# Performance work log

Measured on AMD Instinct MI355X. Metric: run time of the kernel, lower is better.

## Reference

```python
import jax, jax.numpy as jnp
import numpy as np

D_MODEL = 1024
NUM_HEADS = 16
D_K = D_MODEL // NUM_HEADS


def setup_inputs() -> dict:
    key = jax.random.key(0)
    ks = jax.random.split(key, 9)
    B, S = 4, 2048
    s = 1.0 / np.sqrt(D_MODEL)
    inp = {
        "x": jax.random.normal(ks[0], (B, S, D_MODEL), dtype=jnp.float32),
        "wq": jax.random.uniform(ks[1], (D_MODEL, D_MODEL), jnp.float32, -s, s),
        "bq": jax.random.uniform(ks[2], (D_MODEL,), jnp.float32, -s, s),
        "wk": jax.random.uniform(ks[3], (D_MODEL, D_MODEL), jnp.float32, -s, s),
        "bk": jax.random.uniform(ks[4], (D_MODEL,), jnp.float32, -s, s),
        "wv": jax.random.uniform(ks[5], (D_MODEL, D_MODEL), jnp.float32, -s, s),
        "bv": jax.random.uniform(ks[6], (D_MODEL,), jnp.float32, -s, s),
        "wo": jax.random.uniform(ks[7], (D_MODEL, D_MODEL), jnp.float32, -s, s),
        "bo": jax.random.uniform(ks[8], (D_MODEL,), jnp.float32, -s, s),
    }
    return inp


def reference(x, wq, bq, wk, bk, wv, bv, wo, bo):
    B, S, _ = x.shape
    H, Dk = NUM_HEADS, D_K
    # QKV projections; weights stored as (in, out) so y = x @ w + b
    q = (x @ wq + bq).reshape(B, S, H, Dk).transpose(0, 2, 1, 3)  # (B,H,S,Dk)
    k = (x @ wk + bk).reshape(B, S, H, Dk).transpose(0, 2, 1, 3)
    v = (x @ wv + bv).reshape(B, S, H, Dk).transpose(0, 2, 1, 3)
    scores = jnp.einsum("bhqd,bhkd->bhqk", q, k) / jnp.sqrt(jnp.float32(Dk))
    causal = jnp.tril(jnp.ones((S, S), dtype=bool))  # True = keep
    scores = jnp.where(causal, scores, jnp.float32(-jnp.inf))
    attn = jax.nn.softmax(scores, axis=-1)  # dropout=0 (eval)
    out = jnp.einsum("bhqk,bhkd->bhqd", attn, v)
    out = out.transpose(0, 2, 1, 3).reshape(B, S, H * Dk)
    return out @ wo + bo
```

## Files before the change

kernel.cpp:

```cpp
#include <hip/hip_runtime.h>
#include <hip/hip_bf16.h>


#define D_MODEL 1024
#define NHEADS  16
#define DK      64
#define BATCH   4
#define SEQ     2048
#define MROWS   (BATCH*SEQ)

typedef short bvec8 __attribute__((ext_vector_type(8)));
typedef float fvec4 __attribute__((ext_vector_type(4)));

__device__ __forceinline__ unsigned short f2bf(float f) {
    unsigned int x = __float_as_uint(f);
    x += 0x7fffu + ((x >> 16) & 1u);
    return (unsigned short)(x >> 16);
}

__device__ __forceinline__ unsigned pack_bf16x2(float a, float b) {
#if __has_builtin(__builtin_amdgcn_cvt_pk_bf16_f32)
    typedef __bf16 bf16x2_t __attribute__((ext_vector_type(2)));
    union { bf16x2_t v; unsigned u; } cv;
    cv.v = __builtin_amdgcn_cvt_pk_bf16_f32(a, b);
    return cv.u;
#else
    return (unsigned)f2bf(a) | ((unsigned)f2bf(b) << 16);
#endif
}

__device__ __forceinline__ float fast_exp2(float x) {
#if __has_builtin(__builtin_amdgcn_exp2f)
    return __builtin_amdgcn_exp2f(x);
#else
    return exp2f(x);
#endif
}


__global__ void f32_to_bf16_k(const float* __restrict__ in,
                              unsigned short* __restrict__ out, int n4) {
    int i = blockIdx.x * 256 + threadIdx.x;
    if (i < n4) {
        float4 v = ((const float4*)in)[i];
        ushort4 o;
        o.x = f2bf(v.x); o.y = f2bf(v.y); o.z = f2bf(v.z); o.w = f2bf(v.w);
        ((ushort4*)out)[i] = o;
    }
}

__global__ void transpose_all_k(const float* __restrict__ wq, const float* __restrict__ wk,
                                const float* __restrict__ wv, const float* __restrict__ wo,
                                unsigned short* __restrict__ wqkvt,
                                unsigned short* __restrict__ wot) {
    __shared__ float tile[32][33];
    const int z = blockIdx.z;
    const float* W = (z == 0) ? wq : (z == 1) ? wk : (z == 2) ? wv : wo;
    unsigned short* Wt = (z == 3) ? wot : wqkvt + (size_t)z * D_MODEL * D_MODEL;
    int n0 = blockIdx.x * 32, k0 = blockIdx.y * 32;
    int tx = threadIdx.x & 31;
    int ty = (threadIdx.x >> 5) * 4;
#pragma unroll
    for (int i = 0; i < 4; ++i)
        tile[ty + i][tx] = W[(k0 + ty + i) * D_MODEL + n0 + tx];
    __syncthreads();
#pragma unroll
    for (int i = 0; i < 4; ++i)
        Wt[(n0 + ty + i) * D_MODEL + k0 + tx] = f2bf(tile[tx][ty + i]);
}

__global__ void build_cbias_k(const float* __restrict__ bq, const float* __restrict__ bk,
                              const float* __restrict__ bv, float* __restrict__ cb) {
    int i = blockIdx.x * 256 + threadIdx.x;
    float v = (i < 1024) ? bq[i] : (i < 2048) ? bk[i - 1024] : bv[i - 2048];
    cb[i] = v;
}

__global__ __launch_bounds__(256, 4)
void gemm_glds(const unsigned short* __restrict__ A,
               const unsigned short* __restrict__ Bt,
               const float* __restrict__ bias,
               unsigned short* __restrict__ oq,
               unsigned short* __restrict__ ok,
               unsigned short* __restrict__ ov,
               float* __restrict__ of,
               float qscale, int mode) {
    __shared__ __align__(16) unsigned short As[128 * 64];
    __shared__ __align__(16) unsigned short Bs[128 * 64];

    const int tid  = threadIdx.x;
    const int lane = tid & 63;
    const int w    = tid >> 6;
    const int wr   = w >> 1, wc = w & 1;
    const int quad = lane >> 4, l16 = lane & 15;
    const int rowBlock = blockIdx.y * 128;
    const int colBlock = blockIdx.x * 128;

    const int lrow   = lane >> 3;
    const int gchunk = (lane & 7) ^ lrow;

    fvec4 acc[4][4] = {};

    for (int k0 = 0; k0 < D_MODEL; k0 += 64) {
        __syncthreads();
#pragma unroll
        for (int n = 0; n < 4; ++n) {
            const int g = w * 4 + n;
            const int ra = rowBlock + g * 8 + lrow;
            const int ca = colBlock + g * 8 + lrow;
            __builtin_amdgcn_global_load_lds(
                (const __attribute__((address_space(1))) void*)
                    &A[(size_t)ra * D_MODEL + k0 + gchunk * 8],
                (__attribute__((address_space(3))) void*)&As[g * 512], 16, 0, 0);
            __builtin_amdgcn_global_load_lds(
                (const __attribute__((address_space(1))) void*)
                    &Bt[(size_t)ca * D_MODEL + k0 + gchunk * 8],
                (__attribute__((address_space(3))) void*)&Bs[g * 512], 16, 0, 0);
        }
        __syncthreads();
#pragma unroll
        for (int kc = 0; kc < 2; ++kc) {
            bvec8 af[4], bfr[4];
#pragma unroll
            for (int i = 0; i < 4; ++i) {
                int r = wr * 64 + i * 16 + l16;
                af[i] = *(const bvec8*)&As[r * 64 + (((kc * 4 + quad) ^ (l16 & 7)) * 8)];
            }
#pragma unroll
            for (int j = 0; j < 4; ++j) {
                int r = wc * 64 + j * 16 + l16;
                bfr[j] = *(const bvec8*)&Bs[r * 64 + (((kc * 4 + quad) ^ (l16 & 7)) * 8)];
            }
#pragma unroll
            for (int i = 0; i < 4; ++i)
#pragma unroll
                for (int j = 0; j < 4; ++j)
                    acc[i][j] = __builtin_amdgcn_mfma_f32_16x16x32_bf16(
                        af[i], bfr[j], acc[i][j], 0, 0, 0);
        }
    }

    if (mode == 0) {
#pragma unroll
        for (int i = 0; i < 4; ++i) {
#pragma unroll
            for (int j = 0; j < 4; ++j) {
                int ncol = colBlock + wc * 64 + j * 16 + l16;
                int which = ncol >> 10;
                int nn = ncol & 1023;
                int h = nn >> 6, d = nn & 63;
                float bv = bias[ncol];
#pragma unroll
                for (int r = 0; r < 4; ++r) {
                    int mrow = rowBlock + wr * 64 + i * 16 + quad * 4 + r;
                    int b = mrow >> 11, s = mrow & (SEQ - 1);
                    float v = acc[i][j][r] + bv;
                    if (which == 0)
                        oq[(((b * NHEADS + h) * SEQ + s) * DK) + d] = f2bf(v * qscale);
                    else if (which == 1)
                        ok[(((b * NHEADS + h) * SEQ + s) * DK) + d] = f2bf(v);
                    else
                        ov[(((b * NHEADS + h) * DK + d) * SEQ) + s] = f2bf(v);
                }
            }
        }
    } else {
#pragma unroll
        for (int i = 0; i < 4; ++i) {
#pragma unroll
            for (int j = 0; j < 4; ++j) {
                int ncol = colBlock + wc * 64 + j * 16 + l16;
                float bv = bias[ncol];
#pragma unroll
                for (int r = 0; r < 4; ++r) {
                    int mrow = rowBlock + wr * 64 + i * 16 + quad * 4 + r;
                    of[(size_t)mrow * D_MODEL + ncol] = acc[i][j][r] + bv;
                }
            }
        }
    }
}

__global__ __launch_bounds__(256, 4)
void attn_mfma7(const unsigned short* __restrict__ Q,
                const unsigned short* __restrict__ K,
                const unsigned short* __restrict__ Vt,
                unsigned short* __restrict__ O) {
    __shared__ __align__(16) unsigned short Ksm[2][64 * 64];
    __shared__ __align__(16) unsigned short Vsm[2][64 * 64];
    __shared__ __align__(16) unsigned short Pl[4][32 * 32];

    const int tid  = threadIdx.x;
    const int lane = tid & 63;
    const int wq   = tid >> 6;
    const int quad = lane >> 4, l16 = lane & 15;
    const int bx = blockIdx.x;
    const int qt = (bx & 1) ? ((bx - 1) >> 1) : (15 - (bx >> 1));
    const int h = blockIdx.y, b = blockIdx.z;

    const size_t bhq = ((size_t)b * NHEADS + h) * SEQ * DK;
    const unsigned short* Qb = Q + bhq;
    const unsigned short* Kb = K + bhq;
    const unsigned short* Vb = Vt + bhq;

    const int q0 = qt * 128 + wq * 32;

    bvec8 qf[2][2];
#pragma unroll
    for (int qg = 0; qg < 2; ++qg)
#pragma unroll
        for (int kc = 0; kc < 2; ++kc)
            qf[qg][kc] = *(const bvec8*)&Qb[(q0 + qg * 16 + l16) * DK + kc * 32 + quad * 8];

    const int sr = tid >> 2;
    const int sc = tid & 3;
    const int sp0 = ((sc) ^ (sr & 7)) * 8;
    const int sp1 = ((sc + 4) ^ (sr & 7)) * 8;
    unsigned short* Pw = &Pl[wq][0];

    const int ktmax = 2 * qt + 1;
    const int ktact = 2 * qt + (wq >> 1);
    const int mofs  = (wq & 1) << 5;

    bvec8 kr0, kr1, vr0, vr1;
    {
        const unsigned short* kg = Kb + sr * DK;
        kr0 = *(const bvec8*)(kg + sc * 8);
        kr1 = *(const bvec8*)(kg + (sc + 4) * 8);
        const unsigned short* vg = Vb + sr * SEQ;
        vr0 = *(const bvec8*)(vg + sc * 8);
        vr1 = *(const bvec8*)(vg + (sc + 4) * 8);
        *(bvec8*)&Ksm[0][sr * 64 + sp0] = kr0;
        *(bvec8*)&Ksm[0][sr * 64 + sp1] = kr1;
        *(bvec8*)&Vsm[0][sr * 64 + sp0] = vr0;
        *(bvec8*)&Vsm[0][sr * 64 + sp1] = vr1;
    }

    fvec4 acc[2][4] = {};
    float lp[2] = {0.f, 0.f};

    for (int kt = 0; kt <= ktmax; ++kt) {
        __syncthreads();
        const int buf = kt & 1;
        if (kt < ktmax) {
            const unsigned short* kg = Kb + ((kt + 1) * 64 + sr) * DK;
            kr0 = *(const bvec8*)(kg + sc * 8);
            kr1 = *(const bvec8*)(kg + (sc + 4) * 8);
            const unsigned short* vg = Vb + sr * SEQ + (kt + 1) * 64;
            vr0 = *(const bvec8*)(vg + sc * 8);
            vr1 = *(const bvec8*)(vg + (sc + 4) * 8);
        }
        if (kt <= ktact) {
            const unsigned short* Kbuf = &Ksm[buf][0];
            const unsigned short* Vbuf = &Vsm[buf][0];
#pragma unroll
            for (int half = 0; half < 2; ++half) {
#pragma unroll
                for (int tl = 0; tl < 2; ++tl) {
                    const int t4 = half * 2 + tl;
                    fvec4 s[2] = {};
#pragma unroll
                    for (int kc = 0; kc < 2; ++kc) {
                        bvec8 af = *(const bvec8*)
                            &Kbuf[(t4 * 16 + l16) * 64 + (((kc * 4 + quad) ^ (l16 & 7)) * 8)];
#pragma unroll
                        for (int qg = 0; qg < 2; ++qg)
                            s[qg] = __builtin_amdgcn_mfma_f32_16x16x32_bf16(
                                af, qf[qg][kc], s[qg], 0, 0, 0);
                    }
                    if (kt == ktact) {
#pragma unroll
                        for (int qg = 0; qg < 2; ++qg)
#pragma unroll
                            for (int r = 0; r < 4; ++r) {
                                int key = t4 * 16 + quad * 4 + r - mofs;
                                int qq  = qg * 16 + l16;
                                if (key > qq) s[qg][r] = -__builtin_inff();
                            }
                    }
#pragma unroll
                    for (int qg = 0; qg < 2; ++qg) {
                        float p0 = fast_exp2(s[qg][0]);
                        float p1 = fast_exp2(s[qg][1]);
                        float p2 = fast_exp2(s[qg][2]);
                        float p3 = fast_exp2(s[qg][3]);
                        lp[qg] += (p0 + p1) + (p2 + p3);
                        uint2 pk;
                        pk.x = pack_bf16x2(p0, p1);
                        pk.y = pack_bf16x2(p2, p3);
                        *(uint2*)&Pw[(qg * 16 + l16) * 32 +
                                     (((tl * 2 + (quad >> 1)) ^ (l16 & 3)) * 8) +
                                     (quad & 1) * 4] = pk;
                    }
                }
                bvec8 ap[2];
#pragma unroll
                for (int qg = 0; qg < 2; ++qg)
                    ap[qg] = *(const bvec8*)
                        &Pw[(qg * 16 + l16) * 32 + ((quad ^ (l16 & 3)) * 8)];
#pragma unroll
                for (int dt = 0; dt < 4; ++dt) {
                    bvec8 bv = *(const bvec8*)
                        &Vbuf[(dt * 16 + l16) * 64 + (((half * 4 + quad) ^ (l16 & 7)) * 8)];
#pragma unroll
                    for (int qg = 0; qg < 2; ++qg)
                        acc[qg][dt] = __builtin_amdgcn_mfma_f32_16x16x32_bf16(
                            ap[qg], bv, acc[qg][dt], 0, 0, 0);
                }
            }
        }
        if (kt < ktmax) {
            const int nb = buf ^ 1;
            *(bvec8*)&Ksm[nb][sr * 64 + sp0] = kr0;
            *(bvec8*)&Ksm[nb][sr * 64 + sp1] = kr1;
            *(bvec8*)&Vsm[nb][sr * 64 + sp0] = vr0;
            *(bvec8*)&Vsm[nb][sr * 64 + sp1] = vr1;
        }
    }

#pragma unroll
    for (int qg = 0; qg < 2; ++qg) {
        float lr = lp[qg];
        lr += __shfl_xor(lr, 16);
        lr += __shfl_xor(lr, 32);
        float invv[4];
#pragma unroll
        for (int r = 0; r < 4; ++r)
            invv[r] = 1.f / __shfl(lr, quad * 4 + r);
#pragma unroll
        for (int r = 0; r < 4; ++r) {
            size_t row = (size_t)(b * SEQ + q0 + qg * 16 + quad * 4 + r);
            unsigned short* dst = O + row * D_MODEL + h * DK + l16;
#pragma unroll
            for (int dt = 0; dt < 4; ++dt)
                dst[dt * 16] = f2bf(acc[qg][dt][r] * invv[r]);
        }
    }
}


extern "C" void kernel_launch(void* const* d_in, const int* in_sizes, int n_in,
                              void* d_out, int out_size, void* d_ws, size_t ws_size,
                              hipStream_t stream) {
    const float* x  = (const float*)d_in[0];
    const float* wq = (const float*)d_in[1];
    const float* bq = (const float*)d_in[2];
    const float* wk = (const float*)d_in[3];
    const float* bk = (const float*)d_in[4];
    const float* wv = (const float*)d_in[5];
    const float* bv = (const float*)d_in[6];
    const float* wo = (const float*)d_in[7];
    const float* bo = (const float*)d_in[8];
    float* out = (float*)d_out;

    char* ws = (char*)d_ws;
    const size_t MB = 1u << 20;
    unsigned short* xb    = (unsigned short*)(ws);
    unsigned short* wqkvt = (unsigned short*)(ws + 16 * MB);
    unsigned short* wot   = (unsigned short*)(ws + 22 * MB);
    unsigned short* qb    = (unsigned short*)(ws + 24 * MB);
    unsigned short* kb    = (unsigned short*)(ws + 40 * MB);
    unsigned short* vtb   = (unsigned short*)(ws + 56 * MB);
    unsigned short* ab    = (unsigned short*)(ws + 72 * MB);
    float* cbias = (float*)(ws + 72 * MB);

    f32_to_bf16_k<<<(MROWS * D_MODEL / 4 + 255) / 256, 256, 0, stream>>>(
        x, xb, MROWS * D_MODEL / 4);
    transpose_all_k<<<dim3(32, 32, 4), 256, 0, stream>>>(wq, wk, wv, wo, wqkvt, wot);
    build_cbias_k<<<12, 256, 0, stream>>>(bq, bk, bv, cbias);

    const float QSCALE = 0.125f * 1.44269504088896340736f;

    gemm_glds<<<dim3(3072 / 128, MROWS / 128), 256, 0, stream>>>(
        xb, wqkvt, cbias, qb, kb, vtb, nullptr, QSCALE, 0);

    attn_mfma7<<<dim3(SEQ / 128, NHEADS, BATCH), 256, 0, stream>>>(qb, kb, vtb, ab);

    gemm_glds<<<dim3(D_MODEL / 128, MROWS / 128), 256, 0, stream>>>(
        ab, wot, bo, nullptr, nullptr, nullptr, out, 1.0f, 1);
}
```

Measured before the change: 318.4 us.

## Switch attention kernel to 32x32x16 MFMA with register-shuffled P operand

Rewrites the attention inner loop to use 32x32x16 bf16 MFMA tiles instead of 16x16x32. Computing S^T lets the probability tile be rearranged into the A operand of the PV product through cross-half lane shuffles, so the per-wave LDS staging buffer for P and its writes and reads go away. The softmax denominator is now reduced through a small shared array in the epilogue. This cuts LDS traffic and MFMA instruction count, but adds shuffle and select work and more accumulator registers, which may reduce occupancy.

```diff
diff --git a/kernel.cpp b/kernel.cpp
--- a/kernel.cpp
+++ b/kernel.cpp
@@ -10,7 +10,8 @@
 #define MROWS   (BATCH*SEQ)
 
 typedef short bvec8 __attribute__((ext_vector_type(8)));
-typedef float fvec4 __attribute__((ext_vector_type(4)));
+typedef float fvec4  __attribute__((ext_vector_type(4)));
+typedef float fvec16 __attribute__((ext_vector_type(16)));
 
 __device__ __forceinline__ unsigned short f2bf(float f) {
     unsigned int x = __float_as_uint(f);
@@ -182,41 +183,39 @@
 }
 
 __global__ __launch_bounds__(256, 4)
-void attn_mfma7(const unsigned short* __restrict__ Q,
+void attn_mfma8(const unsigned short* __restrict__ Q,
                 const unsigned short* __restrict__ K,
                 const unsigned short* __restrict__ Vt,
                 unsigned short* __restrict__ O) {
     __shared__ __align__(16) unsigned short Ksm[2][64 * 64];
     __shared__ __align__(16) unsigned short Vsm[2][64 * 64];
-    __shared__ __align__(16) unsigned short Pl[4][32 * 32];
+    __shared__ float Lsh[4][32];
 
     const int tid  = threadIdx.x;
     const int lane = tid & 63;
     const int wq   = tid >> 6;
-    const int quad = lane >> 4, l16 = lane & 15;
+    const int hf   = lane >> 5;
+    const int l32  = lane & 31;
     const int bx = blockIdx.x;
     const int qt = (bx & 1) ? ((bx - 1) >> 1) : (15 - (bx >> 1));
-    const int h = blockIdx.y, b = blockIdx.z;
-
-    const size_t bhq = ((size_t)b * NHEADS + h) * SEQ * DK;
+    const int hh = blockIdx.y, b = blockIdx.z;
+
+    const size_t bhq = ((size_t)b * NHEADS + hh) * SEQ * DK;
     const unsigned short* Qb = Q + bhq;
     const unsigned short* Kb = K + bhq;
     const unsigned short* Vb = Vt + bhq;
 
     const int q0 = qt * 128 + wq * 32;
 
-    bvec8 qf[2][2];
-#pragma unroll
-    for (int qg = 0; qg < 2; ++qg)
-#pragma unroll
-        for (int kc = 0; kc < 2; ++kc)
-            qf[qg][kc] = *(const bvec8*)&Qb[(q0 + qg * 16 + l16) * DK + kc * 32 + quad * 8];
+    bvec8 qf[4];
+#pragma unroll
+    for (int kc = 0; kc < 4; ++kc)
+        qf[kc] = *(const bvec8*)&Qb[(q0 + l32) * DK + kc * 16 + hf * 8];
 
     const int sr = tid >> 2;
     const int sc = tid & 3;
     const int sp0 = ((sc) ^ (sr & 7)) * 8;
     const int sp1 = ((sc + 4) ^ (sr & 7)) * 8;
-    unsigned short* Pw = &Pl[wq][0];
 
     const int ktmax = 2 * qt + 1;
     const int ktact = 2 * qt + (wq >> 1);
@@ -236,8 +235,9 @@
         *(bvec8*)&Vsm[0][sr * 64 + sp1] = vr1;
     }
 
-    fvec4 acc[2][4] = {};
-    float lp[2] = {0.f, 0.f};
+    fvec16 acc0 = {};
+    fvec16 acc1 = {};
+    float lp = 0.f;
 
     for (int kt = 0; kt <= ktmax; ++kt) {
         __syncthreads();
@@ -253,60 +253,55 @@
         if (kt <= ktact) {
             const unsigned short* Kbuf = &Ksm[buf][0];
             const unsigned short* Vbuf = &Vsm[buf][0];
-#pragma unroll
-            for (int half = 0; half < 2; ++half) {
-#pragma unroll
-                for (int tl = 0; tl < 2; ++tl) {
-                    const int t4 = half * 2 + tl;
-                    fvec4 s[2] = {};
-#pragma unroll
-                    for (int kc = 0; kc < 2; ++kc) {
-                        bvec8 af = *(const bvec8*)
-                            &Kbuf[(t4 * 16 + l16) * 64 + (((kc * 4 + quad) ^ (l16 & 7)) * 8)];
-#pragma unroll
-                        for (int qg = 0; qg < 2; ++qg)
-                            s[qg] = __builtin_amdgcn_mfma_f32_16x16x32_bf16(
-                                af, qf[qg][kc], s[qg], 0, 0, 0);
-                    }
-                    if (kt == ktact) {
-#pragma unroll
-                        for (int qg = 0; qg < 2; ++qg)
-#pragma unroll
-                            for (int r = 0; r < 4; ++r) {
-                                int key = t4 * 16 + quad * 4 + r - mofs;
-                                int qq  = qg * 16 + l16;
-                                if (key > qq) s[qg][r] = -__builtin_inff();
-                            }
-                    }
-#pragma unroll
-                    for (int qg = 0; qg < 2; ++qg) {
-                        float p0 = fast_exp2(s[qg][0]);
-                        float p1 = fast_exp2(s[qg][1]);
-                        float p2 = fast_exp2(s[qg][2]);
-                        float p3 = fast_exp2(s[qg][3]);
-                        lp[qg] += (p0 + p1) + (p2 + p3);
-                        uint2 pk;
-                        pk.x = pack_bf16x2(p0, p1);
-                        pk.y = pack_bf16x2(p2, p3);
-                        *(uint2*)&Pw[(qg * 16 + l16) * 32 +
-                                     (((tl * 2 + (quad >> 1)) ^ (l16 & 3)) * 8) +
-                                     (quad & 1) * 4] = pk;
-                    }
+
+            fvec16 s0 = {}, s1 = {};
+#pragma unroll
+            for (int kc = 0; kc < 4; ++kc) {
+                const int ch = (((kc * 2 + hf) ^ (l32 & 7)) * 8);
+                bvec8 a0 = *(const bvec8*)&Kbuf[l32 * 64 + ch];
+                bvec8 a1 = *(const bvec8*)&Kbuf[(32 + l32) * 64 + ch];
+                s0 = __builtin_amdgcn_mfma_f32_32x32x16_bf16(a0, qf[kc], s0, 0, 0, 0);
+                s1 = __builtin_amdgcn_mfma_f32_32x32x16_bf16(a1, qf[kc], s1, 0, 0, 0);
+            }
+
+            if (kt == ktact) {
+#pragma unroll
+                for (int r = 0; r < 16; ++r) {
+                    const int key0 = (r & 3) + 8 * (r >> 2) + 4 * hf - mofs;
+                    if (key0 > l32)      s0[r] = -__builtin_inff();
+                    if (key0 + 32 > l32) s1[r] = -__builtin_inff();
                 }
-                bvec8 ap[2];
-#pragma unroll
-                for (int qg = 0; qg < 2; ++qg)
-                    ap[qg] = *(const bvec8*)
-                        &Pw[(qg * 16 + l16) * 32 + ((quad ^ (l16 & 3)) * 8)];
-#pragma unroll
-                for (int dt = 0; dt < 4; ++dt) {
-                    bvec8 bv = *(const bvec8*)
-                        &Vbuf[(dt * 16 + l16) * 64 + (((half * 4 + quad) ^ (l16 & 7)) * 8)];
-#pragma unroll
-                    for (int qg = 0; qg < 2; ++qg)
-                        acc[qg][dt] = __builtin_amdgcn_mfma_f32_16x16x32_bf16(
-                            ap[qg], bv, acc[qg][dt], 0, 0, 0);
-                }
+            }
+
+            unsigned pk[16];
+#pragma unroll
+            for (int m = 0; m < 8; ++m) {
+                float p0 = fast_exp2(s0[2 * m]);
+                float p1 = fast_exp2(s0[2 * m + 1]);
+                float p2 = fast_exp2(s1[2 * m]);
+                float p3 = fast_exp2(s1[2 * m + 1]);
+                lp += (p0 + p1) + (p2 + p3);
+                pk[m]     = pack_bf16x2(p0, p1);
+                pk[8 + m] = pack_bf16x2(p2, p3);
+            }
+
+#pragma unroll
+            for (int kc16 = 0; kc16 < 4; ++kc16) {
+                const int b0 = (kc16 >> 1) * 8 + (kc16 & 1) * 4;
+                unsigned sw0 = __shfl_xor(pk[b0 + 0], 32);
+                unsigned sw1 = __shfl_xor(pk[b0 + 1], 32);
+                unsigned sw2 = __shfl_xor(pk[b0 + 2], 32);
+                unsigned sw3 = __shfl_xor(pk[b0 + 3], 32);
+                union { unsigned u[4]; bvec8 v; } afu;
+                afu.u[0] = hf ? sw2 : pk[b0 + 0];
+                afu.u[1] = hf ? sw3 : pk[b0 + 1];
+                afu.u[2] = hf ? pk[b0 + 2] : sw0;
+                afu.u[3] = hf ? pk[b0 + 3] : sw1;
+                const int ch = (((kc16 * 2 + hf) ^ (l32 & 7)) * 8);
+                bvec8 bv0 = *(const bvec8*)&Vbuf[l32 * 64 + ch];
+                bvec8 bv1 = *(const bvec8*)&Vbuf[(32 + l32) * 64 + ch];
+                acc0 = __builtin_amdgcn_mfma_f32_32x32x16_bf16(afu.v, bv0, acc0, 0, 0, 0);
+                acc1 = __builtin_amdgcn_mfma_f32_32x32x16_bf16(afu.v, bv1, acc1, 0, 0, 0);
             }
         }
         if (kt < ktmax) {
@@ -318,22 +313,21 @@
         }
     }
 
-#pragma unroll
-    for (int qg = 0; qg < 2; ++qg) {
-        float lr = lp[qg];
-        lr += __shfl_xor(lr, 16);
-        lr += __shfl_xor(lr, 32);
-        float invv[4];
-#pragma unroll
-        for (int r = 0; r < 4; ++r)
-            invv[r] = 1.f / __shfl(lr, quad * 4 + r);
-#pragma unroll
-        for (int r = 0; r < 4; ++r) {
-            size_t row = (size_t)(b * SEQ + q0 + qg * 16 + quad * 4 + r);
-            unsigned short* dst = O + row * D_MODEL + h * DK + l16;
-#pragma unroll
-            for (int dt = 0; dt < 4; ++dt)
-                dst[dt * 16] = f2bf(acc[qg][dt][r] * invv[r]);
+    {
+        float l = lp + __shfl_xor(lp, 32);
+        if (lane < 32) Lsh[wq][l32] = l;
+    }
+#pragma unroll
+    for (int g = 0; g < 4; ++g) {
+        float4 lv = *(const float4*)&Lsh[wq][g * 8 + 4 * hf];
+#pragma unroll
+        for (int rr = 0; rr < 4; ++rr) {
+            const int reg = g * 4 + rr;
+            const int qrow = q0 + g * 8 + 4 * hf + rr;
+            const float inv = 1.f / ((const float*)&lv)[rr];
+            unsigned short* dst = O + (size_t)(b * SEQ + qrow) * D_MODEL + hh * DK + l32;
+            dst[0]  = f2bf(acc0[reg] * inv);
+            dst[32] = f2bf(acc1[reg] * inv);
         }
     }
 }
@@ -374,7 +368,7 @@
     gemm_glds<<<dim3(3072 / 128, MROWS / 128), 256, 0, stream>>>(
         xb, wqkvt, cbias, qb, kb, vtb, nullptr, QSCALE, 0);
 
-    attn_mfma7<<<dim3(SEQ / 128, NHEADS, BATCH), 256, 0, stream>>>(qb, kb, vtb, ab);
+    attn_mfma8<<<dim3(SEQ / 128, NHEADS, BATCH), 256, 0, stream>>>(qb, kb, vtb, ab);
 
     gemm_glds<<<dim3(D_MODEL / 128, MROWS / 128), 256, 0, stream>>>(
         ab, wot, bo, nullptr, nullptr, nullptr, out, 1.0f, 1);
```

After: 315.7 us. Within noise of the previous version (-0.8%).
